# Performance work log

Hardware: AMD Instinct MI355X
Metric: run time of the kernel (lower is better)

The kernel has to match this reference:

```python
import jax, jax.numpy as jnp
import numpy as np

B, D, L = 16, 256, 200
T = 1000   # max_frame_length
K = 3      # kernel_size
DW, DC = 4, 2


def setup_inputs() -> dict:
    key = jax.random.key(0)
    ks = jax.random.split(key, 16)
    plen = jax.random.randint(ks[0], (B,), 150, L + 1)
    pm = jnp.arange(L)[None, :] < plen[:, None]              # (B,L) True=valid
    phoneme_mask = pm[:, None, :]                            # (B,1,L)
    durations = jax.random.uniform(ks[1], (B, L), minval=1.0, maxval=8.0) * pm
    phoneme = jax.random.normal(ks[2], (B, D, L), dtype=jnp.float32)
    s = 0.05
    params = {
        'Wpw': jax.random.normal(ks[3], (D, D)) * s, 'bpw': jnp.zeros((D,)),
        'Cw': jax.random.normal(ks[4], (8, D, K)) * s, 'cbw': jnp.zeros((8,)),
        'Mw': jax.random.normal(ks[5], (10, DW)) * s, 'mbw': jnp.zeros((DW,)),
        'Lw': jax.random.normal(ks[6], (DW * D, D)) * s, 'lbw': jnp.zeros((D,)),
        'Wpc': jax.random.normal(ks[7], (D, D)) * s, 'bpc': jnp.zeros((D,)),
        'Cc': jax.random.normal(ks[8], (8, D, K)) * s, 'cbc': jnp.zeros((8,)),
        'Mc': jax.random.normal(ks[9], (10, DC)) * s, 'mbc': jnp.zeros((DC,)),
        'Lc': jax.random.normal(ks[10], (DW * DC, D)) * s, 'lbc': jnp.zeros((D,)),
        'Wo': jax.random.normal(ks[11], (D, 2 * D)) * s, 'bo': jnp.zeros((2 * D,)),
    }
    return {'durations': durations, 'phoneme': phoneme, 'phoneme_mask': phoneme_mask, **params}


def _conv_swish(x, W1, b1, Ck, cb, pm):
    # 1x1 conv (proj) then kernel-K 'same' conv then SiLU; mask padded phones
    h = jnp.einsum('od,bdl->bol', W1, x) + b1[None, :, None]
    h = jax.lax.conv_general_dilated(h, Ck, (1,), 'SAME',
                                     dimension_numbers=('NCH', 'OIH', 'NCH')) + cb[None, :, None]
    h = jax.nn.silu(h)
    h = jnp.where(pm[:, None, :], h, 0.0)
    return h.transpose(0, 2, 1)  # (B, L, 8)


def _mlp(S, E, h, M, mb):
    # concat start/end boundary scalars with per-phone conv features -> (B,T,L,10)
    feat = jnp.concatenate([S[..., None], E[..., None],
                            jnp.broadcast_to(h[:, None], (B, T, L, 8))], axis=-1)
    return jax.nn.silu(feat @ M + mb)


def _forward(durations, phoneme, phoneme_mask, Wpw, bpw, Cw, cbw, Mw, mbw, Lw, lbw,
             Wpc, bpc, Cc, cbc, Mc, mbc, Lc, lbc, Wo, bo):
    pm = phoneme_mask[:, 0, :]                                          # (B,L)
    frame_lengths = jnp.clip(jnp.round(durations.sum(-1)).astype(jnp.int32), 0, T)
    frame_mask = jnp.arange(T)[None, :] < frame_lengths[:, None]        # (B,T)
    attn_mask = frame_mask[:, :, None] & pm[:, None, :]                 # (B,T,L)
    sd = jnp.cumsum(durations, axis=-1)                                 # (B,L)
    sk = sd - durations
    t = jnp.arange(1, T + 1, dtype=durations.dtype)
    S = jnp.where(attn_mask, t[None, :, None] - sk[:, None, :], 0.0)    # (B,T,L)
    E = jnp.where(attn_mask, (sd - sk)[:, None, :], 0.0)                # (B,T,L)

    h_w = _conv_swish(phoneme, Wpw, bpw, Cw, cbw, pm)
    w = _mlp(S, E, h_w, Mw, mbw)                                        # (B,T,L,DW)
    w = jnp.where(pm[:, None, :, None], w, -jnp.inf)
    w = jax.nn.softmax(w, axis=2)                                       # softmax over phones
    w = jnp.where(frame_mask[:, :, None, None], w, 0.0)

    h_c = _conv_swish(phoneme, Wpc, bpc, Cc, cbc, pm)
    c = _mlp(S, E, h_c, Mc, mbc)                                        # (B,T,L,DC)

    wh = jnp.einsum('btlq,bdl->btqd', w, phoneme).reshape(B, T, DW * D) @ Lw + lbw
    wc = jnp.einsum('btlq,btlp->btqp', w, c).reshape(B, T, DW * DC) @ Lc + lbc
    whc = jnp.where(frame_mask[..., None], wh + wc, 0.0)                # (B,T,D)
    out = (whc @ Wo + bo).transpose(0, 2, 1)                            # (B,2D,T)
    return out, frame_mask, frame_lengths, w.transpose(0, 3, 1, 2)


def reference(durations, phoneme, phoneme_mask, Wpw, bpw, Cw, cbw, Mw, mbw, Lw, lbw,
              Wpc, bpc, Cc, cbc, Mc, mbc, Lc, lbc, Wo, bo):
    out, frame_mask, frame_lengths, w = _forward(
        durations, phoneme, phoneme_mask, Wpw, bpw, Cw, cbw, Mw, mbw, Lw, lbw,
        Wpc, bpc, Cc, cbc, Mc, mbc, Lc, lbc, Wo, bo)
    mean, log_std = jnp.split(out, 2, axis=1)                           # (B,D,T) each
    return (mean, log_std, frame_mask, frame_lengths, w)
```

## Files before the change

### kernel.cpp

```cpp
#include <hip/hip_runtime.h>
#include <hip/hip_bf16.h>
#include <math.h>

#define NB 16
#define ND 256
#define NL 200
#define NT 1000

typedef unsigned short ushort_t;
typedef __bf16 bf16x8 __attribute__((ext_vector_type(8)));
typedef float f32x4 __attribute__((ext_vector_type(4)));

#define OFF_PHT   0u
#define OFF_SK    4966400u
#define OFF_EW    4969600u
#define OFF_EC    4975744u
#define OFF_BW2   4981888u
#define OFF_BC2   4981912u
#define OFF_FL    4981936u
#define OFF_GT    11535552u
#define OFF_WOT   15221952u
#define OFF_BASE  15287488u
#define OFF_PHTB  15320256u
#define OFF_LWT   15844544u

__device__ __forceinline__ float silu_f(float x){ return x / (1.f + __expf(-x)); }
__device__ __forceinline__ ushort_t f2bf(float x){
  __hip_bfloat16 h = __float2bfloat16(x);
  return *(ushort_t*)&h;
}

__global__ __launch_bounds__(256) void k_stage1(
    const float* __restrict__ dur, const float* __restrict__ ph,
    const float* __restrict__ Wp_w, const float* __restrict__ C_w, const float* __restrict__ bp_w,
    const float* __restrict__ Wp_c, const float* __restrict__ C_c, const float* __restrict__ bp_c,
    const float* __restrict__ Wo, const float* __restrict__ Lw,
    float* __restrict__ sk_ws, int* __restrict__ fl_ws,
    float* __restrict__ o_fm, float* __restrict__ o_fl,
    float* __restrict__ Ew, float* __restrict__ Ec,
    float* __restrict__ bw2, float* __restrict__ bc2,
    ushort_t* __restrict__ WoT, ushort_t* __restrict__ LwT,
    float* __restrict__ phT, ushort_t* __restrict__ phTb)
{
  int bid = blockIdx.x, tid = threadIdx.x;
  if (bid < 16){
    int b = bid;
    __shared__ float sdur[NL];
    __shared__ float ssk[NL];
    __shared__ int sfl;
    if (tid < NL) sdur[tid] = dur[b*NL + tid];
    __syncthreads();
    if (tid == 0){
      float run = 0.f;
      for (int l = 0; l < NL; ++l){ ssk[l] = run; run += sdur[l]; }
      int fl = (int)rintf(run);
      fl = fl < 0 ? 0 : (fl > NT ? NT : fl);
      sfl = fl; fl_ws[b] = fl; o_fl[b] = (float)fl;
    }
    __syncthreads();
    if (tid < NL) sk_ws[b*NL + tid] = ssk[tid];
    for (int t = tid; t < NT; t += 256) o_fm[b*NT + t] = (t < sfl) ? 1.f : 0.f;
  } else if (bid < 1600){
    int sbid = bid - 16;
    if (sbid < 48){
      int gid = sbid*256 + tid;
      int branch = gid / 6144;
      int r = gid % 6144;
      int d = r & 255;
      int ock = r >> 8;
      int oc = ock / 3, k = ock % 3;
      const float* Wp = branch ? Wp_c : Wp_w;
      const float* C  = branch ? C_c  : C_w;
      float acc = 0.f;
      for (int i = 0; i < ND; ++i) acc += C[(oc*ND + i)*3 + k] * Wp[i*ND + d];
      (branch ? Ec : Ew)[r] = acc;
      if (d == 0){
        const float* bp = branch ? bp_c : bp_w;
        float bb = 0.f;
        for (int i = 0; i < ND; ++i) bb += C[(oc*ND + i)*3 + k] * bp[i];
        (branch ? bc2 : bw2)[ock] = bb;
      }
    } else {
      int gid = (sbid - 48)*256 + tid;
      if (gid < 131072){
        int n = gid >> 8, k = gid & 255;
        WoT[gid] = f2bf(Wo[(size_t)k*512 + n]);
      } else {
        int r = gid - 131072;
        int d = r & 255;
        int qn = r >> 8;
        int q = qn >> 8, n = qn & 255;
        LwT[r] = f2bf(Lw[((size_t)q*256 + d)*256 + n]);
      }
    }
  } else {
    int r = bid - 1600;
    int xb = r & 7, yb = (r >> 3) & 7, b = r >> 6;
    int l0 = xb*32, d0 = yb*32;
    int tx = tid & 31, ty = tid >> 5;
    __shared__ float tile[32][33];
    #pragma unroll
    for (int i = 0; i < 4; ++i){
      int d = d0 + ty + i*8, l = l0 + tx;
      tile[ty + i*8][tx] = (l < NL) ? ph[((size_t)b*ND + d)*NL + l] : 0.f;
    }
    __syncthreads();
    #pragma unroll
    for (int i = 0; i < 4; ++i){
      int l = l0 + ty + i*8, d = d0 + tx;
      float v = tile[tx][ty + i*8];
      if (l < NL) phT[((size_t)b*NL + l)*ND + d] = v;
      phTb[((size_t)b*256 + l)*ND + d] = f2bf(v);
    }
  }
}

__global__ __launch_bounds__(256) void k_stage2(
    const float* __restrict__ phT,
    const float* __restrict__ dur, const float* __restrict__ sk_ws,
    const float* __restrict__ Ew, const float* __restrict__ Ec,
    const float* __restrict__ bw2, const float* __restrict__ bc2,
    const float* __restrict__ cbw, const float* __restrict__ cbc,
    const float* __restrict__ Mw, const float* __restrict__ mbw,
    const float* __restrict__ Mc, const float* __restrict__ mbc,
    float4* __restrict__ base,
    const ushort_t* __restrict__ LwT, const ushort_t* __restrict__ phTb,
    ushort_t* __restrict__ Gt)
{
  __shared__ __align__(16) unsigned char smem[128*136*2];
  int bid = blockIdx.x, tid = threadIdx.x;
  if (bid < 256){
    int b = bid >> 4, x = bid & 15;
    if (x >= 13){
      int l0 = 208 + (x - 13)*16;
      if (tid < 32)
        base[((size_t)(b*256 + l0 + (tid >> 1)))*2 + (tid & 1)] = make_float4(0,0,0,0);
      return;
    }
    float (*sh)[17] = (float (*)[17])smem;
    int lu = tid >> 4, u = tid & 15;
    int l = x*16 + lu;
    float h = 0.f;
    if (l < NL){
      int branch = u >> 3, oc = u & 7;
      const float* E  = branch ? Ec  : Ew;
      const float* b2 = branch ? bc2 : bw2;
      float val = (branch ? cbc : cbw)[oc];
      #pragma unroll
      for (int k = 0; k < 3; ++k){
        int ll = l + k - 1;
        if (ll < 0 || ll >= NL) continue;
        float acc = b2[oc*3 + k];
        const float4* Er = (const float4*)(E + (oc*3 + k)*ND);
        const float4* pr = (const float4*)(phT + ((size_t)b*NL + ll)*ND);
        #pragma unroll 8
        for (int d = 0; d < 64; ++d){
          float4 e = Er[d], p = pr[d];
          acc += e.x*p.x + e.y*p.y + e.z*p.z + e.w*p.w;
        }
        val += acc;
      }
      float pm = (dur[b*NL + l] > 0.5f) ? 1.f : 0.f;
      h = silu_f(val) * pm;
    }
    sh[lu][u] = h;
    __syncthreads();
    if (tid < 16){
      int ll = x*16 + tid;
      float4 o0 = make_float4(0,0,0,0);
      float4 o1 = make_float4(0,0,0,0);
      if (ll < NL){
        float dl  = dur[b*NL + ll];
        float pm  = (dl > 0.5f) ? 1.f : 0.f;
        float skl = sk_ws[b*NL + ll];
        float c1[4], c2[2];
        #pragma unroll
        for (int q = 0; q < 4; ++q) c1[q] = mbw[q] + dl*Mw[4 + q] - skl*Mw[q];
        #pragma unroll
        for (int p = 0; p < 2; ++p) c2[p] = mbc[p] + dl*Mc[2 + p] - skl*Mc[p];
        #pragma unroll
        for (int j = 0; j < 8; ++j){
          float hwv = sh[tid][j], hcv = sh[tid][8 + j];
          #pragma unroll
          for (int q = 0; q < 4; ++q) c1[q] += hwv*Mw[(2 + j)*4 + q];
          #pragma unroll
          for (int p = 0; p < 2; ++p) c2[p] += hcv*Mc[(2 + j)*2 + p];
        }
        o0 = make_float4(c1[0], c1[1], c1[2], c1[3]);
        o1 = make_float4(c2[0], c2[1], pm, 0.f);
      }
      base[((size_t)(b*256 + ll))*2 + 0] = o0;
      base[((size_t)(b*256 + ll))*2 + 1] = o1;
    }
  } else {
    int r = bid - 256;
    int xb = r & 1, yb = (r >> 1) & 1, bq = r >> 2;
    int b = bq >> 2, q = bq & 3;
    int m0 = yb * 128;
    int n0 = xb * 128;
    int lane = tid & 63, wave = tid >> 6;
    int wm = wave >> 1, wn = wave & 1;
    int col = lane & 15, kg4 = lane >> 4;
    f32x4 acc[4][4] = {};
    for (int kt = 0; kt < 8; ++kt){
      int k0 = kt*32;
      bf16x8 afr[4], bfr[4];
      #pragma unroll
      for (int i = 0; i < 4; ++i)
        afr[i] = *(const bf16x8*)(LwT + ((size_t)(q*256 + m0 + wm*64 + i*16 + col))*256 + k0 + kg4*8);
      #pragma unroll
      for (int j = 0; j < 4; ++j)
        bfr[j] = *(const bf16x8*)(phTb + ((size_t)(b*256 + n0 + wn*64 + j*16 + col))*256 + k0 + kg4*8);
      #pragma unroll
      for (int i = 0; i < 4; ++i)
        #pragma unroll
        for (int j = 0; j < 4; ++j)
          acc[i][j] = __builtin_amdgcn_mfma_f32_16x16x32_bf16(afr[i], bfr[j], acc[i][j], 0, 0, 0);
    }
    ushort_t (*st2)[136] = (ushort_t (*)[136])smem;
    int rq = lane >> 4;
    #pragma unroll
    for (int i = 0; i < 4; ++i){
      #pragma unroll
      for (int rr = 0; rr < 4; ++rr){
        int rl = wm*64 + i*16 + rq*4 + rr;
        #pragma unroll
        for (int j = 0; j < 4; ++j){
          int cl = wn*64 + j*16 + col;
          st2[rl][cl] = f2bf(acc[i][j][rr]);
        }
      }
    }
    __syncthreads();
    #pragma unroll
    for (int rep = 0; rep < 8; ++rep){
      int row = rep*16 + (tid >> 4);
      int ch  = tid & 15;
      int l   = n0 + ch*8;
      if (l < NL){
        int n = m0 + row;
        *(uint4*)(Gt + ((size_t)(b*ND + n))*800 + q*NL + l) = *(const uint4*)&st2[row][ch*8];
      }
    }
  }
}

#define AP 808
#define TT 64
__global__ __launch_bounds__(1024, 4) void k_wv_fused(
    const float4* __restrict__ base,
    const int* __restrict__ fl_ws,
    const float* __restrict__ Mw, const float* __restrict__ Mc,
    const ushort_t* __restrict__ Gt,
    const float* __restrict__ Lc,
    const float* __restrict__ lbc,
    const float* __restrict__ lbw,
    const ushort_t* __restrict__ WoT,
    const float* __restrict__ bo,
    float* __restrict__ wout,
    float* __restrict__ o_mean, float* __restrict__ o_lstd)
{
  __shared__ ushort_t As[TT*AP];
  __shared__ float    wcs[TT][8];
  int b = blockIdx.x;
  int m0 = blockIdx.y * TT;
  int tid = threadIdx.x, lane = tid & 63, wave = tid >> 6;
  int col = lane & 15, kg4 = lane >> 4;
  int fl = fl_ws[b];

  if (fl <= m0){
    for (int idx = tid; idx < TT*4*50; idx += 1024){
      int tl = idx / 200;
      int rqs = idx - tl*200;
      int q = rqs / 50, seg = rqs - q*50;
      int t = m0 + tl;
      if (t < NT)
        *(float4*)&wout[(((size_t)(b*4 + q))*NT + t)*NL + seg*4] = make_float4(0,0,0,0);
    }
    for (int idx = tid; idx < 512*16; idx += 1024){
      int s = idx >> 4, j = idx & 15;
      int t0 = m0 + j*4;
      if (t0 + 3 < NT){
        float v = bo[s];
        float4 v4 = make_float4(v, v, v, v);
        if (s < ND) *(float4*)&o_mean[((size_t)b*ND + s)*NT + t0] = v4;
        else        *(float4*)&o_lstd[((size_t)b*ND + (s - ND))*NT + t0] = v4;
      }
    }
    return;
  }

  for (int s = 0; s < 4; ++s){
    int tl = wave*4 + s;
    int t = m0 + tl;
    if (t >= fl){
      for (int k = lane; k < 800; k += 64) As[tl*AP + k] = 0;
      if (lane < 8) wcs[tl][lane] = 0.f;
      if (t < NT){
        float4 z4 = make_float4(0,0,0,0);
        #pragma unroll
        for (int q = 0; q < 4; ++q)
          if (lane < 50)
            *(float4*)&wout[(((size_t)(b*4 + q))*NT + t)*NL + lane*4] = z4;
      }
      continue;
    }
    float t1 = (float)(t + 1);
    float tqw[4], tqc[2];
    #pragma unroll
    for (int q = 0; q < 4; ++q) tqw[q] = t1 * Mw[q];
    #pragma unroll
    for (int p = 0; p < 2; ++p) tqc[p] = t1 * Mc[p];
    float z[4][4], cv[4][2], msk[4];
    float m[4] = {-INFINITY, -INFINITY, -INFINITY, -INFINITY};
    #pragma unroll
    for (int c = 0; c < 4; ++c){
      int l = c*64 + lane;
      float4 b0 = base[((size_t)(b*256 + l))*2 + 0];
      float4 b1 = base[((size_t)(b*256 + l))*2 + 1];
      float pm = b1.z;
      msk[c] = pm;
      float zz[4] = { b0.x + tqw[0], b0.y + tqw[1], b0.z + tqw[2], b0.w + tqw[3] };
      #pragma unroll
      for (int q = 0; q < 4; ++q){
        float sv = silu_f(zz[q]);
        z[c][q] = (pm > 0.f) ? sv : -INFINITY;
        m[q] = fmaxf(m[q], z[c][q]);
      }
      cv[c][0] = silu_f(b1.x + tqc[0]);
      cv[c][1] = silu_f(b1.y + tqc[1]);
    }
    #pragma unroll
    for (int q = 0; q < 4; ++q){
      float v = m[q];
      #pragma unroll
      for (int off = 32; off; off >>= 1) v = fmaxf(v, __shfl_xor(v, off));
      m[q] = v;
    }
    float s4[4] = {0,0,0,0};
    #pragma unroll
    for (int c = 0; c < 4; ++c){
      #pragma unroll
      for (int q = 0; q < 4; ++q){
        float e = (msk[c] > 0.f) ? __expf(z[c][q] - m[q]) : 0.f;
        z[c][q] = e;
        s4[q] += e;
      }
    }
    #pragma unroll
    for (int q = 0; q < 4; ++q){
      float v = s4[q];
      #pragma unroll
      for (int off = 32; off; off >>= 1) v += __shfl_xor(v, off);
      s4[q] = 1.f / v;
    }
    float wc[8] = {0,0,0,0,0,0,0,0};
    #pragma unroll
    for (int c = 0; c < 4; ++c){
      int l = c*64 + lane;
      bool lv = l < NL;
      #pragma unroll
      for (int q = 0; q < 4; ++q){
        float wq = z[c][q] * s4[q];
        if (lv){
          wout[(((size_t)(b*4 + q))*NT + t)*NL + l] = wq;
          As[tl*AP + q*NL + l] = f2bf(wq);
        }
        wc[q*2 + 0] += wq * cv[c][0];
        wc[q*2 + 1] += wq * cv[c][1];
      }
    }
    #pragma unroll
    for (int u = 0; u < 8; ++u){
      float v = wc[u];
      #pragma unroll
      for (int off = 32; off; off >>= 1) v += __shfl_xor(v, off);
      wc[u] = v;
    }
    if (lane == 0){
      #pragma unroll
      for (int u = 0; u < 8; ++u) wcs[tl][u] = wc[u];
    }
  }
  __syncthreads();

  f32x4 acc[4] = {};
  const ushort_t* Gb = Gt + (size_t)b*ND*800;
  for (int kt = 0; kt < 25; ++kt){
    int k0 = kt*32;
    bf16x8 afr[4], bfr;
    #pragma unroll
    for (int i = 0; i < 4; ++i)
      afr[i] = *(const bf16x8*)(&As[(i*16 + col)*AP + k0 + kg4*8]);
    bfr = *(const bf16x8*)(Gb + ((size_t)(wave*16 + col))*800 + k0 + kg4*8);
    #pragma unroll
    for (int i = 0; i < 4; ++i)
      acc[i] = __builtin_amdgcn_mfma_f32_16x16x32_bf16(afr[i], bfr, acc[i], 0, 0, 0);
  }
  __syncthreads();

  ushort_t (*stc)[264] = (ushort_t (*)[264])As;
  {
    int rq = lane >> 4;
    int n = wave*16 + col;
    float lbn = lbc[n], lbwn = lbw[n];
    float lcn[8];
    #pragma unroll
    for (int u = 0; u < 8; ++u) lcn[u] = Lc[u*ND + n];
    #pragma unroll
    for (int i = 0; i < 4; ++i){
      #pragma unroll
      for (int r = 0; r < 4; ++r){
        int tl = i*16 + rq*4 + r;
        int t = m0 + tl;
        if (t < NT){
          float f = (t < fl) ? 1.f : 0.f;
          float vcv = lbn
            + wcs[tl][0]*lcn[0] + wcs[tl][1]*lcn[1]
            + wcs[tl][2]*lcn[2] + wcs[tl][3]*lcn[3]
            + wcs[tl][4]*lcn[4] + wcs[tl][5]*lcn[5]
            + wcs[tl][6]*lcn[6] + wcs[tl][7]*lcn[7];
          stc[tl][n] = f2bf(f * (acc[i][r] + lbwn + vcv));
        }
      }
    }
  }
  __syncthreads();

  {
    f32x4 acc2[2][4] = {};
    for (int kt = 0; kt < 8; ++kt){
      int k0 = kt*32;
      bf16x8 afr[2], bfr[4];
      #pragma unroll
      for (int j = 0; j < 4; ++j)
        bfr[j] = *(const bf16x8*)(&stc[j*16 + col][k0 + kg4*8]);
      #pragma unroll
      for (int i = 0; i < 2; ++i)
        afr[i] = *(const bf16x8*)(WoT + ((size_t)(wave*32 + i*16 + col))*ND + k0 + kg4*8);
      #pragma unroll
      for (int i = 0; i < 2; ++i)
        #pragma unroll
        for (int j = 0; j < 4; ++j)
          acc2[i][j] = __builtin_amdgcn_mfma_f32_16x16x32_bf16(afr[i], bfr[j], acc2[i][j], 0, 0, 0);
    }
    int rq = lane >> 4;
    #pragma unroll
    for (int i = 0; i < 2; ++i){
      #pragma unroll
      for (int r = 0; r < 4; ++r){
        int s = wave*32 + i*16 + rq*4 + r;
        float bov = bo[s];
        #pragma unroll
        for (int j = 0; j < 4; ++j){
          int t = m0 + j*16 + col;
          if (t < NT){
            float v = acc2[i][j][r] + bov;
            if (s < ND) o_mean[((size_t)b*ND + s)*NT + t] = v;
            else        o_lstd[((size_t)b*ND + (s - ND))*NT + t] = v;
          }
        }
      }
    }
  }
}

extern "C" void kernel_launch(void* const* d_in, const int* in_sizes, int n_in,
                              void* d_out, int out_size, void* d_ws, size_t ws_size,
                              hipStream_t stream)
{
  const float* dur = (const float*)d_in[0];
  const float* ph  = (const float*)d_in[1];
  const float* Wpw = (const float*)d_in[3];
  const float* bpw = (const float*)d_in[4];
  const float* Cw  = (const float*)d_in[5];
  const float* cbw = (const float*)d_in[6];
  const float* Mw  = (const float*)d_in[7];
  const float* mbw = (const float*)d_in[8];
  const float* Lw  = (const float*)d_in[9];
  const float* lbw = (const float*)d_in[10];
  const float* Wpc = (const float*)d_in[11];
  const float* bpc = (const float*)d_in[12];
  const float* Cc  = (const float*)d_in[13];
  const float* cbc = (const float*)d_in[14];
  const float* Mc  = (const float*)d_in[15];
  const float* mbc = (const float*)d_in[16];
  const float* Lc  = (const float*)d_in[17];
  const float* lbc = (const float*)d_in[18];
  const float* Wo  = (const float*)d_in[19];
  const float* bo  = (const float*)d_in[20];

  float* out    = (float*)d_out;
  float* o_mean = out;
  float* o_lstd = out + (size_t)NB*ND*NT;
  float* o_fm   = o_lstd + (size_t)NB*ND*NT;
  float* o_fl   = o_fm + NB*NT;
  float* o_w    = o_fl + NB;

  float* ws   = (float*)d_ws;
  float* phT  = ws + OFF_PHT;
  float* sk   = ws + OFF_SK;
  float* Ew   = ws + OFF_EW;
  float* Ec   = ws + OFF_EC;
  float* bw2  = ws + OFF_BW2;
  float* bc2  = ws + OFF_BC2;
  int*   fl   = (int*)(ws + OFF_FL);
  ushort_t* Gt   = (ushort_t*)(ws + OFF_GT);
  ushort_t* WoT  = (ushort_t*)(ws + OFF_WOT);
  float4*   base = (float4*)(ws + OFF_BASE);
  ushort_t* phTb = (ushort_t*)(ws + OFF_PHTB);
  ushort_t* LwT  = (ushort_t*)(ws + OFF_LWT);

  k_stage1<<<2624, 256, 0, stream>>>(dur, ph, Wpw, Cw, bpw, Wpc, Cc, bpc, Wo, Lw,
                                     sk, fl, o_fm, o_fl, Ew, Ec, bw2, bc2,
                                     WoT, LwT, phT, phTb);
  k_stage2<<<512, 256, 0, stream>>>(phT, dur, sk, Ew, Ec, bw2, bc2, cbw, cbc,
                                    Mw, mbw, Mc, mbc, base, LwT, phTb, Gt);
  {
    dim3 g(NB, 16);
    k_wv_fused<<<g, 1024, 0, stream>>>(base, fl, Mw, Mc, Gt, Lc, lbc, lbw,
                                       WoT, bo, o_w, o_mean, o_lstd);
  }
}
```

Measured before the change: 234.5 us.

## Vectorize per-lane phone ownership and process two frames per softmax pass

The attention-softmax stage now gives each lane four contiguous phones instead of a strided set. Weights go out as float4 to the output and as packed bf16 pairs to LDS. Per-phone base features are loaded once into registers before the frame loop instead of being reloaded for every frame. Two frames are computed together so their cross-lane reductions and exp work can interleave. The cost is higher register pressure and extra work on an inactive second frame at the boundary.

```diff
diff --git a/kernel.cpp b/kernel.cpp
--- a/kernel.cpp
+++ b/kernel.cpp
@@ -290,96 +290,145 @@
     return;
   }
 
+  int l0 = lane*4;
+  bool lv = (l0 < NL);
+
+  #pragma unroll
   for (int s = 0; s < 4; ++s){
-    int tl = wave*4 + s;
-    int t = m0 + tl;
-    if (t >= fl){
-      for (int k = lane; k < 800; k += 64) As[tl*AP + k] = 0;
-      if (lane < 8) wcs[tl][lane] = 0.f;
-      if (t < NT){
-        float4 z4 = make_float4(0,0,0,0);
-        #pragma unroll
-        for (int q = 0; q < 4; ++q)
-          if (lane < 50)
-            *(float4*)&wout[(((size_t)(b*4 + q))*NT + t)*NL + lane*4] = z4;
-      }
-      continue;
-    }
-    float t1 = (float)(t + 1);
-    float tqw[4], tqc[2];
-    #pragma unroll
-    for (int q = 0; q < 4; ++q) tqw[q] = t1 * Mw[q];
-    #pragma unroll
-    for (int p = 0; p < 2; ++p) tqc[p] = t1 * Mc[p];
-    float z[4][4], cv[4][2], msk[4];
-    float m[4] = {-INFINITY, -INFINITY, -INFINITY, -INFINITY};
-    #pragma unroll
-    for (int c = 0; c < 4; ++c){
-      int l = c*64 + lane;
-      float4 b0 = base[((size_t)(b*256 + l))*2 + 0];
-      float4 b1 = base[((size_t)(b*256 + l))*2 + 1];
-      float pm = b1.z;
-      msk[c] = pm;
-      float zz[4] = { b0.x + tqw[0], b0.y + tqw[1], b0.z + tqw[2], b0.w + tqw[3] };
+    int tl = wave*4 + s, t = m0 + tl;
+    if (t < fl) continue;
+    for (int k = l0; k < 800; k += 256){
+      uint2 zz2; zz2.x = 0u; zz2.y = 0u;
+      *(uint2*)&As[tl*AP + k] = zz2;
+    }
+    if (lane < 8) wcs[tl][lane] = 0.f;
+    if (t < NT && lv){
+      float4 z4 = make_float4(0,0,0,0);
+      #pragma unroll
+      for (int q = 0; q < 4; ++q)
+        *(float4*)&wout[(((size_t)(b*4 + q))*NT + t)*NL + l0] = z4;
+    }
+  }
+
+  float b0a[4][4], b1x[4], b1y[4], pmv[4];
+  #pragma unroll
+  for (int e = 0; e < 4; ++e){
+    float4 v0 = make_float4(0,0,0,0), v1 = make_float4(0,0,0,0);
+    if (lv){
+      v0 = base[((size_t)(b*256 + l0 + e))*2 + 0];
+      v1 = base[((size_t)(b*256 + l0 + e))*2 + 1];
+    }
+    b0a[e][0] = v0.x; b0a[e][1] = v0.y; b0a[e][2] = v0.z; b0a[e][3] = v0.w;
+    b1x[e] = v1.x; b1y[e] = v1.y; pmv[e] = v1.z;
+  }
+  float mwq[4] = {Mw[0], Mw[1], Mw[2], Mw[3]};
+  float mcp[2] = {Mc[0], Mc[1]};
+
+  for (int sp = 0; sp < 2; ++sp){
+    int tl0 = wave*4 + sp*2;
+    int t0 = m0 + tl0;
+    if (t0 >= fl) break;
+    bool a1 = (t0 + 1 < fl);
+    float tf[2] = {(float)(t0 + 1), (float)(t0 + 2)};
+
+    float z[2][4][4], mx[2][4];
+    #pragma unroll
+    for (int u = 0; u < 2; ++u)
+      #pragma unroll
+      for (int q = 0; q < 4; ++q) mx[u][q] = -INFINITY;
+    #pragma unroll
+    for (int e = 0; e < 4; ++e){
+      #pragma unroll
+      for (int u = 0; u < 2; ++u){
+        #pragma unroll
+        for (int q = 0; q < 4; ++q){
+          float sv = silu_f(b0a[e][q] + tf[u]*mwq[q]);
+          float zv = (pmv[e] > 0.f) ? sv : -INFINITY;
+          z[u][e][q] = zv;
+          mx[u][q] = fmaxf(mx[u][q], zv);
+        }
+      }
+    }
+    #pragma unroll
+    for (int u = 0; u < 2; ++u)
       #pragma unroll
       for (int q = 0; q < 4; ++q){
-        float sv = silu_f(zz[q]);
-        z[c][q] = (pm > 0.f) ? sv : -INFINITY;
-        m[q] = fmaxf(m[q], z[c][q]);
-      }
-      cv[c][0] = silu_f(b1.x + tqc[0]);
-      cv[c][1] = silu_f(b1.y + tqc[1]);
-    }
-    #pragma unroll
-    for (int q = 0; q < 4; ++q){
-      float v = m[q];
-      #pragma unroll
-      for (int off = 32; off; off >>= 1) v = fmaxf(v, __shfl_xor(v, off));
-      m[q] = v;
-    }
-    float s4[4] = {0,0,0,0};
-    #pragma unroll
-    for (int c = 0; c < 4; ++c){
+        float v = mx[u][q];
+        #pragma unroll
+        for (int off = 32; off; off >>= 1) v = fmaxf(v, __shfl_xor(v, off));
+        mx[u][q] = v;
+      }
+    float is4[2][4] = {{0,0,0,0},{0,0,0,0}};
+    #pragma unroll
+    for (int e = 0; e < 4; ++e){
+      #pragma unroll
+      for (int u = 0; u < 2; ++u){
+        #pragma unroll
+        for (int q = 0; q < 4; ++q){
+          float ev = (pmv[e] > 0.f) ? __expf(z[u][e][q] - mx[u][q]) : 0.f;
+          z[u][e][q] = ev;
+          is4[u][q] += ev;
+        }
+      }
+    }
+    #pragma unroll
+    for (int u = 0; u < 2; ++u)
       #pragma unroll
       for (int q = 0; q < 4; ++q){
-        float e = (msk[c] > 0.f) ? __expf(z[c][q] - m[q]) : 0.f;
-        z[c][q] = e;
-        s4[q] += e;
-      }
-    }
-    #pragma unroll
-    for (int q = 0; q < 4; ++q){
-      float v = s4[q];
-      #pragma unroll
-      for (int off = 32; off; off >>= 1) v += __shfl_xor(v, off);
-      s4[q] = 1.f / v;
-    }
-    float wc[8] = {0,0,0,0,0,0,0,0};
-    #pragma unroll
-    for (int c = 0; c < 4; ++c){
-      int l = c*64 + lane;
-      bool lv = l < NL;
+        float v = is4[u][q];
+        #pragma unroll
+        for (int off = 32; off; off >>= 1) v += __shfl_xor(v, off);
+        is4[u][q] = 1.f / v;
+      }
+    float cv[2][4][2];
+    #pragma unroll
+    for (int e = 0; e < 4; ++e)
+      #pragma unroll
+      for (int u = 0; u < 2; ++u){
+        cv[u][e][0] = silu_f(b1x[e] + tf[u]*mcp[0]);
+        cv[u][e][1] = silu_f(b1y[e] + tf[u]*mcp[1]);
+      }
+    float wc[2][8];
+    #pragma unroll
+    for (int u = 0; u < 2; ++u)
+      #pragma unroll
+      for (int x = 0; x < 8; ++x) wc[u][x] = 0.f;
+    #pragma unroll
+    for (int u = 0; u < 2; ++u){
+      bool act = (u == 0) || a1;
+      int t = t0 + u, tl = tl0 + u;
       #pragma unroll
       for (int q = 0; q < 4; ++q){
-        float wq = z[c][q] * s4[q];
-        if (lv){
-          wout[(((size_t)(b*4 + q))*NT + t)*NL + l] = wq;
-          As[tl*AP + q*NL + l] = f2bf(wq);
-        }
-        wc[q*2 + 0] += wq * cv[c][0];
-        wc[q*2 + 1] += wq * cv[c][1];
-      }
-    }
-    #pragma unroll
-    for (int u = 0; u < 8; ++u){
-      float v = wc[u];
-      #pragma unroll
-      for (int off = 32; off; off >>= 1) v += __shfl_xor(v, off);
-      wc[u] = v;
-    }
-    if (lane == 0){
-      #pragma unroll
-      for (int u = 0; u < 8; ++u) wcs[tl][u] = wc[u];
+        float w0 = z[u][0][q]*is4[u][q];
+        float w1 = z[u][1][q]*is4[u][q];
+        float w2 = z[u][2][q]*is4[u][q];
+        float w3 = z[u][3][q]*is4[u][q];
+        if (act && lv){
+          *(float4*)&wout[(((size_t)(b*4 + q))*NT + t)*NL + l0] =
+              make_float4(w0, w1, w2, w3);
+          uint2 pk;
+          pk.x = (unsigned)f2bf(w0) | ((unsigned)f2bf(w1) << 16);
+          pk.y = (unsigned)f2bf(w2) | ((unsigned)f2bf(w3) << 16);
+          *(uint2*)&As[tl*AP + q*NL + l0] = pk;
+        }
+        wc[u][q*2 + 0] += w0*cv[u][0][0] + w1*cv[u][1][0] + w2*cv[u][2][0] + w3*cv[u][3][0];
+        wc[u][q*2 + 1] += w0*cv[u][0][1] + w1*cv[u][1][1] + w2*cv[u][2][1] + w3*cv[u][3][1];
+      }
+    }
+    #pragma unroll
+    for (int u = 0; u < 2; ++u){
+      if (u == 1 && !a1) break;
+      #pragma unroll
+      for (int x = 0; x < 8; ++x){
+        float v = wc[u][x];
+        #pragma unroll
+        for (int off = 32; off; off >>= 1) v += __shfl_xor(v, off);
+        wc[u][x] = v;
+      }
+      if (lane == 0){
+        #pragma unroll
+        for (int x = 0; x < 8; ++x) wcs[tl0 + u][x] = wc[u][x];
+      }
     }
   }
   __syncthreads();
```

New measurement: 236.8 us (median of 2 runs). About the same (+1.0%).

## Split softmax attention weights into separate high-parallelism kernel before matmul

Applied to the files above, without the earlier changes.

Moves the per-frame softmax over phones out of the fused 256-block kernel into a new kernel with one wave per frame across 4096 blocks, writing bf16 weights and the 8 weighted conv-feature sums to workspace. The matmul kernel then reads those weights straight from global memory instead of shared memory, and its shared footprint shrinks to the output staging tile. The fused kernel launched only 256 blocks, so the softmax phase underfilled the GPU. The split adds a global round trip for the bf16 weights and one extra launch. Softmax stores are also vectorised to float4.

```diff
diff --git a/kernel.cpp b/kernel.cpp
--- a/kernel.cpp
+++ b/kernel.cpp
@@ -12,12 +12,14 @@
 typedef float f32x4 __attribute__((ext_vector_type(4)));
 
 #define OFF_PHT   0u
+#define OFF_WCS   1000000u
 #define OFF_SK    4966400u
 #define OFF_EW    4969600u
 #define OFF_EC    4975744u
 #define OFF_BW2   4981888u
 #define OFF_BC2   4981912u
 #define OFF_FL    4981936u
+#define OFF_WG    4981952u
 #define OFF_GT    11535552u
 #define OFF_WOT   15221952u
 #define OFF_BASE  15287488u
@@ -245,23 +247,136 @@
   }
 }
 
-#define AP 808
-#define TT 64
-__global__ __launch_bounds__(1024, 4) void k_wv_fused(
+__global__ __launch_bounds__(256) void k_softmax(
     const float4* __restrict__ base,
     const int* __restrict__ fl_ws,
     const float* __restrict__ Mw, const float* __restrict__ Mc,
+    float* __restrict__ wout,
+    ushort_t* __restrict__ wG,
+    float* __restrict__ wcs_g)
+{
+  int lane = threadIdx.x & 63, wave = threadIdx.x >> 6;
+  int wid = blockIdx.x*4 + wave;
+  int b = wid >> 10, t = wid & 1023;
+  int fl = fl_ws[b];
+  ushort_t* wrow = wG + ((size_t)(b << 10) + t)*800;
+
+  if (t >= fl){
+    uint4 z16; z16.x = z16.y = z16.z = z16.w = 0u;
+    for (int k = lane; k < 100; k += 64)
+      *(uint4*)&wrow[k*8] = z16;
+    if (lane < 8) wcs_g[((size_t)(b << 10) + t)*8 + lane] = 0.f;
+    if (t < NT && lane < 50){
+      float4 z4 = make_float4(0,0,0,0);
+      #pragma unroll
+      for (int q = 0; q < 4; ++q)
+        *(float4*)&wout[(((size_t)(b*4 + q))*NT + t)*NL + lane*4] = z4;
+    }
+    return;
+  }
+
+  int l0 = lane*4;
+  bool lv = (l0 < NL);
+  float b0a[4][4], b1x[4], b1y[4], pmv[4];
+  #pragma unroll
+  for (int e = 0; e < 4; ++e){
+    float4 v0 = make_float4(0,0,0,0), v1 = make_float4(0,0,0,0);
+    if (lv){
+      v0 = base[((size_t)(b*256 + l0 + e))*2 + 0];
+      v1 = base[((size_t)(b*256 + l0 + e))*2 + 1];
+    }
+    b0a[e][0] = v0.x; b0a[e][1] = v0.y; b0a[e][2] = v0.z; b0a[e][3] = v0.w;
+    b1x[e] = v1.x; b1y[e] = v1.y; pmv[e] = v1.z;
+  }
+  float tf = (float)(t + 1);
+
+  float z[4][4], mx[4] = {-INFINITY, -INFINITY, -INFINITY, -INFINITY};
+  #pragma unroll
+  for (int e = 0; e < 4; ++e){
+    #pragma unroll
+    for (int q = 0; q < 4; ++q){
+      float sv = silu_f(b0a[e][q] + tf*Mw[q]);
+      float zv = (pmv[e] > 0.f) ? sv : -INFINITY;
+      z[e][q] = zv;
+      mx[q] = fmaxf(mx[q], zv);
+    }
+  }
+  #pragma unroll
+  for (int q = 0; q < 4; ++q){
+    float v = mx[q];
+    #pragma unroll
+    for (int off = 32; off; off >>= 1) v = fmaxf(v, __shfl_xor(v, off));
+    mx[q] = v;
+  }
+  float s4[4] = {0,0,0,0};
+  #pragma unroll
+  for (int e = 0; e < 4; ++e){
+    #pragma unroll
+    for (int q = 0; q < 4; ++q){
+      float ev = (pmv[e] > 0.f) ? __expf(z[e][q] - mx[q]) : 0.f;
+      z[e][q] = ev;
+      s4[q] += ev;
+    }
+  }
+  #pragma unroll
+  for (int q = 0; q < 4; ++q){
+    float v = s4[q];
+    #pragma unroll
+    for (int off = 32; off; off >>= 1) v += __shfl_xor(v, off);
+    s4[q] = 1.f / v;
+  }
+  float cv[4][2];
+  #pragma unroll
+  for (int e = 0; e < 4; ++e){
+    cv[e][0] = silu_f(b1x[e] + tf*Mc[0]);
+    cv[e][1] = silu_f(b1y[e] + tf*Mc[1]);
+  }
+  float wc[8] = {0,0,0,0,0,0,0,0};
+  #pragma unroll
+  for (int q = 0; q < 4; ++q){
+    float w0 = z[0][q]*s4[q];
+    float w1 = z[1][q]*s4[q];
+    float w2 = z[2][q]*s4[q];
+    float w3 = z[3][q]*s4[q];
+    if (lv){
+      *(float4*)&wout[(((size_t)(b*4 + q))*NT + t)*NL + l0] =
+          make_float4(w0, w1, w2, w3);
+      uint2 pk;
+      pk.x = (unsigned)f2bf(w0) | ((unsigned)f2bf(w1) << 16);
+      pk.y = (unsigned)f2bf(w2) | ((unsigned)f2bf(w3) << 16);
+      *(uint2*)&wrow[q*NL + l0] = pk;
+    }
+    wc[q*2 + 0] += w0*cv[0][0] + w1*cv[1][0] + w2*cv[2][0] + w3*cv[3][0];
+    wc[q*2 + 1] += w0*cv[0][1] + w1*cv[1][1] + w2*cv[2][1] + w3*cv[3][1];
+  }
+  #pragma unroll
+  for (int x = 0; x < 8; ++x){
+    float v = wc[x];
+    #pragma unroll
+    for (int off = 32; off; off >>= 1) v += __shfl_xor(v, off);
+    wc[x] = v;
+  }
+  if (lane == 0){
+    #pragma unroll
+    for (int x = 0; x < 8; ++x) wcs_g[((size_t)(b << 10) + t)*8 + x] = wc[x];
+  }
+}
+
+#define TT 64
+__global__ __launch_bounds__(1024, 4) void k_wv2(
+    const int* __restrict__ fl_ws,
+    const ushort_t* __restrict__ wG,
     const ushort_t* __restrict__ Gt,
+    const float* __restrict__ wcs_g,
     const float* __restrict__ Lc,
     const float* __restrict__ lbc,
     const float* __restrict__ lbw,
     const ushort_t* __restrict__ WoT,
     const float* __restrict__ bo,
-    float* __restrict__ wout,
     float* __restrict__ o_mean, float* __restrict__ o_lstd)
 {
-  __shared__ ushort_t As[TT*AP];
-  __shared__ float    wcs[TT][8];
+  __shared__ ushort_t stc[TT][264];
+  __shared__ float wcs_l[TT][8];
   int b = blockIdx.x;
   int m0 = blockIdx.y * TT;
   int tid = threadIdx.x, lane = tid & 63, wave = tid >> 6;
@@ -269,14 +384,6 @@
   int fl = fl_ws[b];
 
   if (fl <= m0){
-    for (int idx = tid; idx < TT*4*50; idx += 1024){
-      int tl = idx / 200;
-      int rqs = idx - tl*200;
-      int q = rqs / 50, seg = rqs - q*50;
-      int t = m0 + tl;
-      if (t < NT)
-        *(float4*)&wout[(((size_t)(b*4 + q))*NT + t)*NL + seg*4] = make_float4(0,0,0,0);
-    }
     for (int idx = tid; idx < 512*16; idx += 1024){
       int s = idx >> 4, j = idx & 15;
       int t0 = m0 + j*4;
@@ -290,108 +397,20 @@
     return;
   }
 
-  for (int s = 0; s < 4; ++s){
-    int tl = wave*4 + s;
-    int t = m0 + tl;
-    if (t >= fl){
-      for (int k = lane; k < 800; k += 64) As[tl*AP + k] = 0;
-      if (lane < 8) wcs[tl][lane] = 0.f;
-      if (t < NT){
-        float4 z4 = make_float4(0,0,0,0);
-        #pragma unroll
-        for (int q = 0; q < 4; ++q)
-          if (lane < 50)
-            *(float4*)&wout[(((size_t)(b*4 + q))*NT + t)*NL + lane*4] = z4;
-      }
-      continue;
-    }
-    float t1 = (float)(t + 1);
-    float tqw[4], tqc[2];
-    #pragma unroll
-    for (int q = 0; q < 4; ++q) tqw[q] = t1 * Mw[q];
-    #pragma unroll
-    for (int p = 0; p < 2; ++p) tqc[p] = t1 * Mc[p];
-    float z[4][4], cv[4][2], msk[4];
-    float m[4] = {-INFINITY, -INFINITY, -INFINITY, -INFINITY};
-    #pragma unroll
-    for (int c = 0; c < 4; ++c){
-      int l = c*64 + lane;
-      float4 b0 = base[((size_t)(b*256 + l))*2 + 0];
-      float4 b1 = base[((size_t)(b*256 + l))*2 + 1];
-      float pm = b1.z;
-      msk[c] = pm;
-      float zz[4] = { b0.x + tqw[0], b0.y + tqw[1], b0.z + tqw[2], b0.w + tqw[3] };
-      #pragma unroll
-      for (int q = 0; q < 4; ++q){
-        float sv = silu_f(zz[q]);
-        z[c][q] = (pm > 0.f) ? sv : -INFINITY;
-        m[q] = fmaxf(m[q], z[c][q]);
-      }
-      cv[c][0] = silu_f(b1.x + tqc[0]);
-      cv[c][1] = silu_f(b1.y + tqc[1]);
-    }
-    #pragma unroll
-    for (int q = 0; q < 4; ++q){
-      float v = m[q];
-      #pragma unroll
-      for (int off = 32; off; off >>= 1) v = fmaxf(v, __shfl_xor(v, off));
-      m[q] = v;
-    }
-    float s4[4] = {0,0,0,0};
-    #pragma unroll
-    for (int c = 0; c < 4; ++c){
-      #pragma unroll
-      for (int q = 0; q < 4; ++q){
-        float e = (msk[c] > 0.f) ? __expf(z[c][q] - m[q]) : 0.f;
-        z[c][q] = e;
-        s4[q] += e;
-      }
-    }
-    #pragma unroll
-    for (int q = 0; q < 4; ++q){
-      float v = s4[q];
-      #pragma unroll
-      for (int off = 32; off; off >>= 1) v += __shfl_xor(v, off);
-      s4[q] = 1.f / v;
-    }
-    float wc[8] = {0,0,0,0,0,0,0,0};
-    #pragma unroll
-    for (int c = 0; c < 4; ++c){
-      int l = c*64 + lane;
-      bool lv = l < NL;
-      #pragma unroll
-      for (int q = 0; q < 4; ++q){
-        float wq = z[c][q] * s4[q];
-        if (lv){
-          wout[(((size_t)(b*4 + q))*NT + t)*NL + l] = wq;
-          As[tl*AP + q*NL + l] = f2bf(wq);
-        }
-        wc[q*2 + 0] += wq * cv[c][0];
-        wc[q*2 + 1] += wq * cv[c][1];
-      }
-    }
-    #pragma unroll
-    for (int u = 0; u < 8; ++u){
-      float v = wc[u];
-      #pragma unroll
-      for (int off = 32; off; off >>= 1) v += __shfl_xor(v, off);
-      wc[u] = v;
-    }
-    if (lane == 0){
-      #pragma unroll
-      for (int u = 0; u < 8; ++u) wcs[tl][u] = wc[u];
-    }
-  }
-  __syncthreads();
+  if (tid < 512){
+    int tl = tid >> 3, u = tid & 7;
+    wcs_l[tl][u] = wcs_g[((size_t)(b << 10) + m0 + tl)*8 + u];
+  }
 
   f32x4 acc[4] = {};
   const ushort_t* Gb = Gt + (size_t)b*ND*800;
+  const ushort_t* Wb = wG + ((size_t)(b << 10) + m0)*800;
   for (int kt = 0; kt < 25; ++kt){
     int k0 = kt*32;
     bf16x8 afr[4], bfr;
     #pragma unroll
     for (int i = 0; i < 4; ++i)
-      afr[i] = *(const bf16x8*)(&As[(i*16 + col)*AP + k0 + kg4*8]);
+      afr[i] = *(const bf16x8*)(Wb + ((size_t)(i*16 + col))*800 + k0 + kg4*8);
     bfr = *(const bf16x8*)(Gb + ((size_t)(wave*16 + col))*800 + k0 + kg4*8);
     #pragma unroll
     for (int i = 0; i < 4; ++i)
@@ -399,7 +418,6 @@
   }
   __syncthreads();
 
-  ushort_t (*stc)[264] = (ushort_t (*)[264])As;
   {
     int rq = lane >> 4;
     int n = wave*16 + col;
@@ -416,10 +434,10 @@
         if (t < NT){
           float f = (t < fl) ? 1.f : 0.f;
           float vcv = lbn
-            + wcs[tl][0]*lcn[0] + wcs[tl][1]*lcn[1]
-            + wcs[tl][2]*lcn[2] + wcs[tl][3]*lcn[3]
-            + wcs[tl][4]*lcn[4] + wcs[tl][5]*lcn[5]
-            + wcs[tl][6]*lcn[6] + wcs[tl][7]*lcn[7];
+            + wcs_l[tl][0]*lcn[0] + wcs_l[tl][1]*lcn[1]
+            + wcs_l[tl][2]*lcn[2] + wcs_l[tl][3]*lcn[3]
+            + wcs_l[tl][4]*lcn[4] + wcs_l[tl][5]*lcn[5]
+            + wcs_l[tl][6]*lcn[6] + wcs_l[tl][7]*lcn[7];
           stc[tl][n] = f2bf(f * (acc[i][r] + lbwn + vcv));
         }
       }
@@ -499,12 +517,14 @@
 
   float* ws   = (float*)d_ws;
   float* phT  = ws + OFF_PHT;
+  float* wcsg = ws + OFF_WCS;
   float* sk   = ws + OFF_SK;
   float* Ew   = ws + OFF_EW;
   float* Ec   = ws + OFF_EC;
   float* bw2  = ws + OFF_BW2;
   float* bc2  = ws + OFF_BC2;
   int*   fl   = (int*)(ws + OFF_FL);
+  ushort_t* wG   = (ushort_t*)(ws + OFF_WG);
   ushort_t* Gt   = (ushort_t*)(ws + OFF_GT);
   ushort_t* WoT  = (ushort_t*)(ws + OFF_WOT);
   float4*   base = (float4*)(ws + OFF_BASE);
@@ -516,9 +536,10 @@
                                      WoT, LwT, phT, phTb);
   k_stage2<<<512, 256, 0, stream>>>(phT, dur, sk, Ew, Ec, bw2, bc2, cbw, cbc,
                                     Mw, mbw, Mc, mbc, base, LwT, phTb, Gt);
+  k_softmax<<<4096, 256, 0, stream>>>(base, fl, Mw, Mc, o_w, wG, wcsg);
   {
     dim3 g(NB, 16);
-    k_wv_fused<<<g, 1024, 0, stream>>>(base, fl, Mw, Mc, Gt, Lc, lbc, lbw,
-                                       WoT, bo, o_w, o_mean, o_lstd);
+    k_wv2<<<g, 1024, 0, stream>>>(fl, wG, Gt, wcsg, Lc, lbc, lbw,
+                                  WoT, bo, o_mean, o_lstd);
   }
 }
```

After: 260.2 us. +11.0%, slower.
